# Kernel optimization log

Measured on AMD Instinct MI355X. Metric: run time of the kernel, lower is better.

The kernel has to match this reference:

```python
import jax, jax.numpy as jnp
import numpy as np

N = 100000
E = 3200000
D_IN = 256
D_OUT = 256
SMOOTH = 0.5


def setup_inputs() -> dict:
    key = jax.random.key(0)
    k1, k2, k3, k4, k5, k6 = jax.random.split(key, 6)
    x = jax.random.normal(k1, (N, D_IN), dtype=jnp.float32)
    W = jax.random.normal(k2, (D_IN, D_OUT), dtype=jnp.float32) * (1.0 / np.sqrt(D_IN))
    b = jax.random.normal(k3, (D_OUT,), dtype=jnp.float32) * 0.01
    edge_weight = jax.random.uniform(k4, (E,), dtype=jnp.float32)
    edge_row = jax.random.randint(k5, (E,), 0, N, dtype=jnp.int32)
    edge_col = jax.random.randint(k6, (E,), 0, N, dtype=jnp.int32)
    return {"x": x, "W": W, "b": b, "edge_weight": edge_weight,
            "edge_row": edge_row, "edge_col": edge_col}


def reference(x, W, b, edge_weight, edge_row, edge_col):
    # support = Linear(input)
    support = x @ W + b  # [N, D_OUT]
    # A_gcn = adj + I; degrees = column sums of A_gcn (identity contributes +1)
    deg = jax.ops.segment_sum(edge_weight, edge_col, num_segments=N) + 1.0  # [N]
    Dm12 = deg ** -0.5  # D^{-1/2}
    # pre-scale, spmm with A_gcn = adj + I, post-scale
    Y = support * Dm12[:, None]
    Z = jax.ops.segment_sum(edge_weight[:, None] * Y[edge_col], edge_row,
                            num_segments=N) + Y  # +Y is the identity part of A_gcn
    Z = Z * Dm12[:, None]
    # residual blend
    return (Z * SMOOTH + support) / (1.0 + SMOOTH)
```

## Files before the change

kernel.cpp:

```cpp
#include <hip/hip_runtime.h>

#define N_NODES 100000
#define N_EDGES 3200000
#define D 256
#define ELL_W 64
#define NPC_CNT 57344
#define NPART_CNT 2
#define NTOTC 114688
#define NPC_ELL 14336
#define NPART_ELL 8
#define NPC_DEG 57344
#define NPART_DEG 2
#define NSLICE2 128
#define SLICE2_E 25000
#define NSLICE_D 128
#define SLICE_D 25000
#define W_SCALE 32768.0f
#define SMOOTH_A (1.0f/3.0f)
#define SMOOTH_B (2.0f/3.0f)

#define AS1 __attribute__((address_space(1)))
#define AS3 __attribute__((address_space(3)))

typedef __attribute__((ext_vector_type(8))) __bf16 bf16x8;
typedef __attribute__((ext_vector_type(4))) float f32x4;
typedef __attribute__((ext_vector_type(2))) float f32x2;

__device__ __forceinline__ unsigned short f2bf(float f) {
    unsigned int u = __float_as_uint(f);
    u = (u + 0x7FFFu + ((u >> 16) & 1u)) >> 16;
    return (unsigned short)u;
}
__device__ __forceinline__ float bf_lo(unsigned int u) { return __uint_as_float(u << 16); }
__device__ __forceinline__ float bf_hi(unsigned int u) { return __uint_as_float(u & 0xFFFF0000u); }

__device__ __forceinline__ unsigned int cvtpk_bf16(float lo, float hi) {
    unsigned int r;
    asm("v_cvt_pk_bf16_f32 %0, %1, %2" : "=v"(r) : "v"(lo), "v"(hi));
    return r;
}

__device__ __forceinline__ void load_lds16(const void* g, void* l) {
    __builtin_amdgcn_global_load_lds((const AS1 unsigned int*)g, (AS3 unsigned int*)l, 16, 0, 0);
}

__global__ void prep_cw_kernel(const int* __restrict__ ecol, const float* __restrict__ ew,
                               unsigned int* __restrict__ cw) {
    int i = blockIdx.x * 256 + threadIdx.x;
    int e0 = i * 4;
    if (e0 >= N_EDGES) return;
    int4 c = *(const int4*)(ecol + e0);
    float4 w = *(const float4*)(ew + e0);
    uint4 o; unsigned q;
    q = __float2uint_rn(w.x * W_SCALE); if (q > 32767u) q = 32767u; o.x = (unsigned)c.x | (q << 17);
    q = __float2uint_rn(w.y * W_SCALE); if (q > 32767u) q = 32767u; o.y = (unsigned)c.y | (q << 17);
    q = __float2uint_rn(w.z * W_SCALE); if (q > 32767u) q = 32767u; o.z = (unsigned)c.z | (q << 17);
    q = __float2uint_rn(w.w * W_SCALE); if (q > 32767u) q = 32767u; o.w = (unsigned)c.w | (q << 17);
    *(uint4*)(cw + e0) = o;
}

__launch_bounds__(256, 2)
__global__ void cntpart_kernel(const int* __restrict__ erow, unsigned char* __restrict__ cnt_s) {
    __shared__ unsigned int h[NPC_CNT / 4];
    int p = blockIdx.x, s = blockIdx.y;
    int base = p * NPC_CNT;
    for (int i = threadIdx.x; i < NPC_CNT / 4; i += 256) h[i] = 0u;
    __syncthreads();
    int q0 = (s * SLICE2_E) >> 2, q1 = q0 + (SLICE2_E >> 2);
    const int4* r4p = (const int4*)erow;
    for (int q = q0 + threadIdx.x; q < q1; q += 256) {
        int4 r = r4p[q];
        int a;
        a = r.x - base; if ((unsigned)a < NPC_CNT) atomicAdd(&h[a >> 2], 1u << ((a & 3) * 8));
        a = r.y - base; if ((unsigned)a < NPC_CNT) atomicAdd(&h[a >> 2], 1u << ((a & 3) * 8));
        a = r.z - base; if ((unsigned)a < NPC_CNT) atomicAdd(&h[a >> 2], 1u << ((a & 3) * 8));
        a = r.w - base; if ((unsigned)a < NPC_CNT) atomicAdd(&h[a >> 2], 1u << ((a & 3) * 8));
    }
    __syncthreads();
    unsigned int* dst = (unsigned int*)(cnt_s + (size_t)s * NTOTC + base);
    for (int i = threadIdx.x; i < NPC_CNT / 4; i += 256) dst[i] = h[i];
}

__launch_bounds__(256, 2)
__global__ void degpart_kernel(const unsigned int* __restrict__ cw, unsigned char* __restrict__ degp) {
    __shared__ unsigned int h[NPC_DEG / 4];
    int p = blockIdx.x, s = blockIdx.y;
    int base = p * NPC_DEG;
    for (int i = threadIdx.x; i < NPC_DEG / 4; i += 256) h[i] = 0u;
    __syncthreads();
    int q0 = (s * SLICE_D) >> 2, q1 = q0 + (SLICE_D >> 2);
    const uint4* c4p = (const uint4*)cw;
    for (int q = q0 + threadIdx.x; q < q1; q += 256) {
        uint4 v = c4p[q];
        int a; unsigned qw;
        a = (int)(v.x & 0x1FFFFu) - base; qw = ((v.x >> 17) + 512u) >> 10;
        if ((unsigned)a < NPC_DEG) atomicAdd(&h[a >> 2], qw << ((a & 3) * 8));
        a = (int)(v.y & 0x1FFFFu) - base; qw = ((v.y >> 17) + 512u) >> 10;
        if ((unsigned)a < NPC_DEG) atomicAdd(&h[a >> 2], qw << ((a & 3) * 8));
        a = (int)(v.z & 0x1FFFFu) - base; qw = ((v.z >> 17) + 512u) >> 10;
        if ((unsigned)a < NPC_DEG) atomicAdd(&h[a >> 2], qw << ((a & 3) * 8));
        a = (int)(v.w & 0x1FFFFu) - base; qw = ((v.w >> 17) + 512u) >> 10;
        if ((unsigned)a < NPC_DEG) atomicAdd(&h[a >> 2], qw << ((a & 3) * 8));
    }
    __syncthreads();
    unsigned int* dst = (unsigned int*)(degp + (size_t)s * NTOTC + base);
    for (int i = threadIdx.x; i < NPC_DEG / 4; i += 256) dst[i] = h[i];
}

__global__ void scanboth_kernel(unsigned char* __restrict__ cnt_s, int* __restrict__ mcnt,
                                const unsigned char* __restrict__ degp, float* __restrict__ dm12) {
    int r = blockIdx.x * 256 + threadIdx.x;
    if (r >= NTOTC) return;
    unsigned int acc = 0;
#pragma unroll
    for (int s = 0; s < NSLICE2; s++) {
        unsigned int v = cnt_s[(size_t)s * NTOTC + r];
        cnt_s[(size_t)s * NTOTC + r] = (unsigned char)acc;
        acc += v;
    }
    mcnt[r] = (int)acc;
    unsigned int qsum = 0;
#pragma unroll
    for (int s = 0; s < NSLICE_D; s++)
        qsum += degp[(size_t)s * NTOTC + r];
    dm12[r] = rsqrtf(1.0f + (float)qsum * (1.0f / 32.0f));
}

__launch_bounds__(256, 4)
__global__ void ellwrite_kernel(const int* __restrict__ erow, const unsigned int* __restrict__ cw,
                                const unsigned char* __restrict__ off,
                                unsigned int* __restrict__ ell) {
    __shared__ unsigned int h[NPC_ELL / 4];
    int p = blockIdx.x, s = blockIdx.y;
    int base = p * NPC_ELL;
    for (int i = threadIdx.x; i < NPC_ELL / 4; i += 256) h[i] = 0u;
    __syncthreads();
    int q0 = (s * SLICE2_E) >> 2, q1 = q0 + (SLICE2_E >> 2);
    const int4* r4p = (const int4*)erow;
    const uint4* c4p = (const uint4*)cw;
    const unsigned char* offs = off + (size_t)s * NTOTC;
#define PUT(rr, vv) do { \
        int a_ = (rr) - base; \
        if ((unsigned)a_ < NPC_ELL) { \
            int sh_ = (a_ & 3) * 8; \
            unsigned int old_ = atomicAdd(&h[a_ >> 2], 1u << sh_); \
            unsigned int rank_ = (old_ >> sh_) & 0xFFu; \
            unsigned int pos_ = (unsigned int)offs[rr] + rank_; \
            if (pos_ < ELL_W) ell[(size_t)(rr) * ELL_W + pos_] = (vv); \
        } \
    } while (0)
    for (int q = q0 + threadIdx.x; q < q1; q += 256) {
        int4 r = r4p[q];
        uint4 v = c4p[q];
        PUT(r.x, v.x);
        PUT(r.y, v.y);
        PUT(r.z, v.z);
        PUT(r.w, v.w);
    }
#undef PUT
}

__global__ void cvt_wt_kernel(const float* __restrict__ W, unsigned short* __restrict__ wt) {
    int t = blockIdx.x * 256 + threadIdx.x;
    int c = t >> 8, k = t & 255;
    wt[t] = f2bf(W[k * D + c]);
}

__launch_bounds__(256, 4)
__global__ void gemm_kernel(const float* __restrict__ x,
                            const unsigned short* __restrict__ wt,
                            const float* __restrict__ bias, const float* __restrict__ dm12,
                            unsigned short* __restrict__ Yh, unsigned char* __restrict__ Yq,
                            int n) {
    __shared__ __align__(16) float As[128 * 32];
    __shared__ __align__(16) unsigned short Bs[128 * 32];
    int t = threadIdx.x;
    int lane = t & 63, wave = t >> 6;
    int wm = wave >> 1, wn = wave & 1;
    int r0 = blockIdx.x * 128;
    int c0 = blockIdx.y * 128;

    f32x4 zero4 = {0.f, 0.f, 0.f, 0.f};
    f32x4 acc[4][4];
#pragma unroll
    for (int m = 0; m < 4; m++)
#pragma unroll
        for (int nn = 0; nn < 4; nn++) acc[m][nn] = zero4;

    int srow = t >> 2;
    int bseg = (t & 3) ^ ((t >> 3) & 3);
    int skseg = bseg * 8;
    char* bbase = (char*)Bs + wave * 1024;
    int aseg = (lane & 7) ^ (lane >> 3);

    for (int kc = 0; kc < 256; kc += 32) {
#pragma unroll
        for (int i = 0; i < 4; i++) {
            int row_local = (i * 4 + wave) * 8 + (lane >> 3);
            int grow = r0 + row_local;
            if (grow >= n) grow = n - 1;
            load_lds16(x + (size_t)grow * 256 + kc + aseg * 4,
                       (char*)As + (i * 4 + wave) * 1024);
        }
        load_lds16(wt + (size_t)(c0 + srow) * 256 + kc + skseg,      bbase);
        load_lds16(wt + (size_t)(c0 + 64 + srow) * 256 + kc + skseg, bbase + 4096);
        __syncthreads();

        bf16x8 bfrag[4];
        int lr = lane & 15;
        int seg0 = (lane >> 4) * 2;
        int bsegr = lane >> 4;
        union { bf16x8 v; unsigned int u[4]; } afrag[4];
#pragma unroll
        for (int m = 0; m < 4; m++) {
            int row = wm * 64 + m * 16 + lr;
            int rk = row & 7;
            const char* rbase = (const char*)As + row * 128;
            f32x4 a0 = *(const f32x4*)(rbase + ((seg0 ^ rk) << 4));
            f32x4 a1 = *(const f32x4*)(rbase + (((seg0 + 1) ^ rk) << 4));
            afrag[m].u[0] = cvtpk_bf16(a0.x, a0.y);
            afrag[m].u[1] = cvtpk_bf16(a0.z, a0.w);
            afrag[m].u[2] = cvtpk_bf16(a1.x, a1.y);
            afrag[m].u[3] = cvtpk_bf16(a1.z, a1.w);
        }
#pragma unroll
        for (int nn = 0; nn < 4; nn++) {
            int row = wn * 64 + nn * 16 + lr;
            int rk = (row >> 1) & 3;
            bfrag[nn] = *(const bf16x8*)((const char*)Bs + row * 64 + ((bsegr ^ rk) << 4));
        }
#pragma unroll
        for (int m = 0; m < 4; m++)
#pragma unroll
            for (int nn = 0; nn < 4; nn++)
                acc[m][nn] = __builtin_amdgcn_mfma_f32_16x16x32_bf16(afrag[m].v, bfrag[nn], acc[m][nn], 0, 0, 0);
        __syncthreads();
    }

#pragma unroll
    for (int nn = 0; nn < 4; nn++) {
        int col = c0 + wn * 64 + nn * 16 + (lane & 15);
        float bb = bias[col];
#pragma unroll
        for (int m = 0; m < 4; m++) {
            int rbase = r0 + wm * 64 + m * 16 + (lane >> 4) * 4;
            f32x4 v = acc[m][nn];
#pragma unroll
            for (int reg = 0; reg < 4; reg++) {
                int r = rbase + reg;
                if (r < n) {
                    float val = (v[reg] + bb) * dm12[r];
                    Yh[(size_t)r * 256 + col] = f2bf(val);
                    unsigned int pk = (unsigned int)__builtin_amdgcn_cvt_pk_fp8_f32(val, val, 0, false);
                    Yq[(size_t)r * 256 + col] = (unsigned char)(pk & 0xFFu);
                }
            }
        }
    }
}

__launch_bounds__(256)
__global__ void gather_kernel(const unsigned short* __restrict__ Yh,
                              const unsigned int* __restrict__ Yq,
                              const int* __restrict__ cnt, const unsigned int* __restrict__ ell,
                              const float* __restrict__ dm12, float* __restrict__ out, int n) {
    int wid = threadIdx.x >> 6, lane = threadIdx.x & 63;
    int r = __builtin_amdgcn_readfirstlane(blockIdx.x * 4 + wid);
    if (r >= n) return;
    const uint2* Y2 = (const uint2*)Yh;
    uint2 ow = Y2[(size_t)r * 64 + lane];
    float o0 = bf_lo(ow.x), o1 = bf_hi(ow.x), o2 = bf_lo(ow.y), o3 = bf_hi(ow.y);
    float a0 = o0, a1 = o1, a2 = o2, a3 = o3;
    int m = cnt[r]; if (m > ELL_W) m = ELL_W;
    const uint4* ep4 = (const uint4*)(ell + (size_t)r * ELL_W);
    int j = 0;
#define WDEC(v) ((float)((v) >> 17) * (1.0f / W_SCALE))
#define CDEC(v) ((v) & 0x1FFFFu)
#define EDGE(qreg, wreg) do { \
        f32x2 lo_ = __builtin_amdgcn_cvt_pk_f32_fp8((int)(qreg), false); \
        f32x2 hi_ = __builtin_amdgcn_cvt_pk_f32_fp8((int)(qreg), true);  \
        a0 = fmaf((wreg), lo_.x, a0); a1 = fmaf((wreg), lo_.y, a1);      \
        a2 = fmaf((wreg), hi_.x, a2); a3 = fmaf((wreg), hi_.y, a3);      \
    } while (0)
    for (; j + 15 < m; j += 16) {
        uint4 eA = ep4[(j >> 2) + 0];
        uint4 eB = ep4[(j >> 2) + 1];
        uint4 eC = ep4[(j >> 2) + 2];
        uint4 eD = ep4[(j >> 2) + 3];
        unsigned int q0  = Yq[(size_t)CDEC(eA.x) * 64 + lane];
        unsigned int q1  = Yq[(size_t)CDEC(eA.y) * 64 + lane];
        unsigned int q2  = Yq[(size_t)CDEC(eA.z) * 64 + lane];
        unsigned int q3  = Yq[(size_t)CDEC(eA.w) * 64 + lane];
        unsigned int q4  = Yq[(size_t)CDEC(eB.x) * 64 + lane];
        unsigned int q5  = Yq[(size_t)CDEC(eB.y) * 64 + lane];
        unsigned int q6  = Yq[(size_t)CDEC(eB.z) * 64 + lane];
        unsigned int q7  = Yq[(size_t)CDEC(eB.w) * 64 + lane];
        unsigned int q8  = Yq[(size_t)CDEC(eC.x) * 64 + lane];
        unsigned int q9  = Yq[(size_t)CDEC(eC.y) * 64 + lane];
        unsigned int q10 = Yq[(size_t)CDEC(eC.z) * 64 + lane];
        unsigned int q11 = Yq[(size_t)CDEC(eC.w) * 64 + lane];
        unsigned int q12 = Yq[(size_t)CDEC(eD.x) * 64 + lane];
        unsigned int q13 = Yq[(size_t)CDEC(eD.y) * 64 + lane];
        unsigned int q14 = Yq[(size_t)CDEC(eD.z) * 64 + lane];
        unsigned int q15 = Yq[(size_t)CDEC(eD.w) * 64 + lane];
        EDGE(q0,  WDEC(eA.x)); EDGE(q1,  WDEC(eA.y));
        EDGE(q2,  WDEC(eA.z)); EDGE(q3,  WDEC(eA.w));
        EDGE(q4,  WDEC(eB.x)); EDGE(q5,  WDEC(eB.y));
        EDGE(q6,  WDEC(eB.z)); EDGE(q7,  WDEC(eB.w));
        EDGE(q8,  WDEC(eC.x)); EDGE(q9,  WDEC(eC.y));
        EDGE(q10, WDEC(eC.z)); EDGE(q11, WDEC(eC.w));
        EDGE(q12, WDEC(eD.x)); EDGE(q13, WDEC(eD.y));
        EDGE(q14, WDEC(eD.z)); EDGE(q15, WDEC(eD.w));
    }
    for (; j + 7 < m; j += 8) {
        uint4 eA = ep4[(j >> 2) + 0];
        uint4 eB = ep4[(j >> 2) + 1];
        unsigned int q0 = Yq[(size_t)CDEC(eA.x) * 64 + lane];
        unsigned int q1 = Yq[(size_t)CDEC(eA.y) * 64 + lane];
        unsigned int q2 = Yq[(size_t)CDEC(eA.z) * 64 + lane];
        unsigned int q3 = Yq[(size_t)CDEC(eA.w) * 64 + lane];
        unsigned int q4 = Yq[(size_t)CDEC(eB.x) * 64 + lane];
        unsigned int q5 = Yq[(size_t)CDEC(eB.y) * 64 + lane];
        unsigned int q6 = Yq[(size_t)CDEC(eB.z) * 64 + lane];
        unsigned int q7 = Yq[(size_t)CDEC(eB.w) * 64 + lane];
        EDGE(q0, WDEC(eA.x)); EDGE(q1, WDEC(eA.y));
        EDGE(q2, WDEC(eA.z)); EDGE(q3, WDEC(eA.w));
        EDGE(q4, WDEC(eB.x)); EDGE(q5, WDEC(eB.y));
        EDGE(q6, WDEC(eB.z)); EDGE(q7, WDEC(eB.w));
    }
    for (; j + 3 < m; j += 4) {
        uint4 eA = ep4[j >> 2];
        unsigned int q0 = Yq[(size_t)CDEC(eA.x) * 64 + lane];
        unsigned int q1 = Yq[(size_t)CDEC(eA.y) * 64 + lane];
        unsigned int q2 = Yq[(size_t)CDEC(eA.z) * 64 + lane];
        unsigned int q3 = Yq[(size_t)CDEC(eA.w) * 64 + lane];
        EDGE(q0, WDEC(eA.x)); EDGE(q1, WDEC(eA.y));
        EDGE(q2, WDEC(eA.z)); EDGE(q3, WDEC(eA.w));
    }
    for (; j < m; j++) {
        unsigned int ev = ell[(size_t)r * ELL_W + j];
        unsigned int qa = Yq[(size_t)CDEC(ev) * 64 + lane];
        EDGE(qa, WDEC(ev));
    }
#undef EDGE
#undef WDEC
#undef CDEC
    float dm = dm12[r];
    float inv = 1.0f / dm;
    float4 o;
    o.x = (a0 * dm) * SMOOTH_A + (o0 * inv) * SMOOTH_B;
    o.y = (a1 * dm) * SMOOTH_A + (o1 * inv) * SMOOTH_B;
    o.z = (a2 * dm) * SMOOTH_A + (o2 * inv) * SMOOTH_B;
    o.w = (a3 * dm) * SMOOTH_A + (o3 * inv) * SMOOTH_B;
    ((float4*)out)[(size_t)r * 64 + lane] = o;
}

extern "C" void kernel_launch(void* const* d_in, const int* in_sizes, int n_in,
                              void* d_out, int out_size, void* d_ws, size_t ws_size,
                              hipStream_t stream) {
    const float* x    = (const float*)d_in[0];
    const float* W    = (const float*)d_in[1];
    const float* b    = (const float*)d_in[2];
    const float* ew   = (const float*)d_in[3];
    const int*   erow = (const int*)d_in[4];
    const int*   ecol = (const int*)d_in[5];
    float* out = (float*)d_out;
    const int n = N_NODES;

    char* wp = (char*)d_ws;
    int*   mcnt = (int*)wp;   wp += 458752;
    float* dm12 = (float*)wp; wp += 458752;
    unsigned short* wt = (unsigned short*)wp; wp += 131072;
    unsigned int* cw = (unsigned int*)wp; wp += (size_t)N_EDGES * 4;
    unsigned int* ell = (unsigned int*)wp; wp += (size_t)N_NODES * ELL_W * 4;
    char*  rgA  = wp;         wp += (size_t)n * D * 2;
    unsigned short* Yh    = (unsigned short*)rgA;
    unsigned char*  cnt_s = (unsigned char*)rgA;
    char*  rgB  = wp;
    unsigned char* degp = (unsigned char*)rgB;
    unsigned char* Yq   = (unsigned char*)rgB;

    prep_cw_kernel<<<(N_EDGES / 4 + 255) / 256, 256, 0, stream>>>(ecol, ew, cw);
    cntpart_kernel<<<dim3(NPART_CNT, NSLICE2), 256, 0, stream>>>(erow, cnt_s);
    degpart_kernel<<<dim3(NPART_DEG, NSLICE_D), 256, 0, stream>>>(cw, degp);
    scanboth_kernel<<<(NTOTC + 255) / 256, 256, 0, stream>>>(cnt_s, mcnt, degp, dm12);
    ellwrite_kernel<<<dim3(NPART_ELL, NSLICE2), 256, 0, stream>>>(erow, cw, cnt_s, ell);
    cvt_wt_kernel<<<(D * D) / 256, 256, 0, stream>>>(W, wt);
    gemm_kernel<<<dim3(782, 2), 256, 0, stream>>>(x, wt, b, dm12, Yh, Yq, n);
    gather_kernel<<<(n + 3) / 4, 256, 0, stream>>>(Yh, (const unsigned int*)Yq, mcnt, ell, dm12, out, n);
}
```

Measured before the change: 351.5 us.

## Swap MFMA operands to get row-contiguous accumulators and vectorize GEMM epilogue stores

```diff
diff --git a/kernel.cpp b/kernel.cpp
--- a/kernel.cpp
+++ b/kernel.cpp
@@ -7,8 +7,8 @@
 #define NPC_CNT 57344
 #define NPART_CNT 2
 #define NTOTC 114688
-#define NPC_ELL 14336
-#define NPART_ELL 8
+#define NPC_ELL 28672
+#define NPART_ELL 4
 #define NPC_DEG 57344
 #define NPART_DEG 2
 #define NSLICE2 128
@@ -207,10 +207,10 @@
         __syncthreads();
 
         bf16x8 bfrag[4];
+        bf16x8 afrag[4];
         int lr = lane & 15;
         int seg0 = (lane >> 4) * 2;
         int bsegr = lane >> 4;
-        union { bf16x8 v; unsigned int u[4]; } afrag[4];
 #pragma unroll
         for (int m = 0; m < 4; m++) {
             int row = wm * 64 + m * 16 + lr;
@@ -218,10 +218,12 @@
             const char* rbase = (const char*)As + row * 128;
             f32x4 a0 = *(const f32x4*)(rbase + ((seg0 ^ rk) << 4));
             f32x4 a1 = *(const f32x4*)(rbase + (((seg0 + 1) ^ rk) << 4));
-            afrag[m].u[0] = cvtpk_bf16(a0.x, a0.y);
-            afrag[m].u[1] = cvtpk_bf16(a0.z, a0.w);
-            afrag[m].u[2] = cvtpk_bf16(a1.x, a1.y);
-            afrag[m].u[3] = cvtpk_bf16(a1.z, a1.w);
+            union { bf16x8 v; unsigned int u[4]; } af;
+            af.u[0] = cvtpk_bf16(a0.x, a0.y);
+            af.u[1] = cvtpk_bf16(a0.z, a0.w);
+            af.u[2] = cvtpk_bf16(a1.x, a1.y);
+            af.u[3] = cvtpk_bf16(a1.z, a1.w);
+            afrag[m] = af.v;
         }
 #pragma unroll
         for (int nn = 0; nn < 4; nn++) {
@@ -233,27 +235,32 @@
         for (int m = 0; m < 4; m++)
 #pragma unroll
             for (int nn = 0; nn < 4; nn++)
-                acc[m][nn] = __builtin_amdgcn_mfma_f32_16x16x32_bf16(afrag[m].v, bfrag[nn], acc[m][nn], 0, 0, 0);
+                acc[m][nn] = __builtin_amdgcn_mfma_f32_16x16x32_bf16(bfrag[nn], afrag[m], acc[m][nn], 0, 0, 0);
         __syncthreads();
     }
 
 #pragma unroll
-    for (int nn = 0; nn < 4; nn++) {
-        int col = c0 + wn * 64 + nn * 16 + (lane & 15);
-        float bb = bias[col];
-#pragma unroll
-        for (int m = 0; m < 4; m++) {
-            int rbase = r0 + wm * 64 + m * 16 + (lane >> 4) * 4;
-            f32x4 v = acc[m][nn];
-#pragma unroll
-            for (int reg = 0; reg < 4; reg++) {
-                int r = rbase + reg;
-                if (r < n) {
-                    float val = (v[reg] + bb) * dm12[r];
-                    Yh[(size_t)r * 256 + col] = f2bf(val);
-                    unsigned int pk = (unsigned int)__builtin_amdgcn_cvt_pk_fp8_f32(val, val, 0, false);
-                    Yq[(size_t)r * 256 + col] = (unsigned char)(pk & 0xFFu);
-                }
+    for (int m = 0; m < 4; m++) {
+        int r = r0 + wm * 64 + m * 16 + (lane & 15);
+        if (r < n) {
+            float dm = dm12[r];
+#pragma unroll
+            for (int nn = 0; nn < 4; nn++) {
+                int colbase = c0 + wn * 64 + nn * 16 + (lane >> 4) * 4;
+                float4 b4 = *(const float4*)(bias + colbase);
+                f32x4 v = acc[m][nn];
+                float v0 = (v[0] + b4.x) * dm;
+                float v1 = (v[1] + b4.y) * dm;
+                float v2 = (v[2] + b4.z) * dm;
+                float v3 = (v[3] + b4.w) * dm;
+                uint2 hv;
+                hv.x = cvtpk_bf16(v0, v1);
+                hv.y = cvtpk_bf16(v2, v3);
+                *(uint2*)(Yh + (size_t)r * 256 + colbase) = hv;
+                int q = 0;
+                q = __builtin_amdgcn_cvt_pk_fp8_f32(v0, v1, q, false);
+                q = __builtin_amdgcn_cvt_pk_fp8_f32(v2, v3, q, true);
+                *(unsigned int*)(Yq + (size_t)r * 256 + colbase) = (unsigned int)q;
             }
         }
     }
```

Result: faster. 316.2 us (median of 2 runs) (-10.0%).
